# Optimization experiments

Hardware: AMD Instinct MI355X
Metric: run time of the kernel (lower is better)

## Reference

```python
import jax, jax.numpy as jnp
import numpy as np

BLOCK = 128  # block_size in the original module


def weight_dequant(weight, scale):
    # weight: [O, I] fp8 values (simulated float32); scale: [O//BLOCK, I//BLOCK] fp32
    O, I = weight.shape
    w = weight.reshape(O // BLOCK, BLOCK, I // BLOCK, BLOCK)
    w = w * scale[:, None, :, None]
    return w.reshape(O, I)


def setup_inputs() -> dict:
    key = jax.random.key(0)
    k1, k2, k3, k4 = jax.random.split(key, 4)
    B, S, IN, OUT = 2, 2048, 4096, 16384
    x = jax.random.normal(k1, (B, S, IN), dtype=jnp.float32)
    weight = jax.random.normal(k2, (OUT, IN), dtype=jnp.float32)
    scale = jax.random.uniform(k3, (OUT // BLOCK, IN // BLOCK), dtype=jnp.float32, minval=0.01, maxval=0.05)
    bias = jax.random.normal(k4, (OUT,), dtype=jnp.float32)
    return {"x": x, "weight": weight, "scale": scale, "bias": bias}


def reference(x, weight, scale, bias):
    # bf16 gemm_impl path: block-wise dequant of fp8 weight, then F.linear(x, W) + bias
    w = weight_dequant(weight, scale)          # [O, I]
    out = jnp.einsum('bsi,oi->bso', x, w)      # x @ W^T
    return out + bias
```

## Files before the change

kernel.cpp:

```cpp
#include <hip/hip_runtime.h>
#include <hip/hip_bf16.h>

#define M_DIM 4096
#define N_DIM 16384
#define K_DIM 4096

typedef __bf16 bf16x8 __attribute__((ext_vector_type(8)));
typedef float f32x4 __attribute__((ext_vector_type(4)));

__device__ __forceinline__ void gload16(const void* g, void* l) {
    __builtin_amdgcn_global_load_lds((__attribute__((address_space(1))) void*)g,
                                     (__attribute__((address_space(3))) void*)l, 16, 0, 0);
}

__global__ __launch_bounds__(256) void cvt_x_kernel(const float* __restrict__ x,
                                                    __hip_bfloat16* __restrict__ out,
                                                    int ngroups) {
    int i = blockIdx.x * blockDim.x + threadIdx.x;
    int stride = gridDim.x * blockDim.x;
    for (; i < ngroups; i += stride) {
        const float4* p = (const float4*)(x + (size_t)i * 8);
        float4 v0 = p[0];
        float4 v1 = p[1];
        bf16x8 r;
        r[0] = (__bf16)v0.x; r[1] = (__bf16)v0.y; r[2] = (__bf16)v0.z; r[3] = (__bf16)v0.w;
        r[4] = (__bf16)v1.x; r[5] = (__bf16)v1.y; r[6] = (__bf16)v1.z; r[7] = (__bf16)v1.w;
        *(bf16x8*)(out + (size_t)i * 8) = r;
    }
}

__global__ __launch_bounds__(256) void dequant_w_kernel(const float* __restrict__ w,
                                                        const float* __restrict__ scale,
                                                        __hip_bfloat16* __restrict__ out) {
    const int ngroups = N_DIM * (K_DIM / 8);
    int i = blockIdx.x * blockDim.x + threadIdx.x;
    int stride = gridDim.x * blockDim.x;
    for (; i < ngroups; i += stride) {
        int row = i >> 9;
        int cg  = i & 511;
        float s = scale[(row >> 7) * (K_DIM / 128) + (cg >> 4)];
        const float4* p = (const float4*)(w + (size_t)i * 8);
        float4 v0 = p[0];
        float4 v1 = p[1];
        bf16x8 r;
        r[0] = (__bf16)(v0.x * s); r[1] = (__bf16)(v0.y * s);
        r[2] = (__bf16)(v0.z * s); r[3] = (__bf16)(v0.w * s);
        r[4] = (__bf16)(v1.x * s); r[5] = (__bf16)(v1.y * s);
        r[6] = (__bf16)(v1.z * s); r[7] = (__bf16)(v1.w * s);
        *(bf16x8*)(out + (size_t)i * 8) = r;
    }
}

__global__ __launch_bounds__(512, 2)
void gemm_bf16_kernel(const __hip_bfloat16* __restrict__ A,
                      const __hip_bfloat16* __restrict__ Bw,
                      const float* __restrict__ bias,
                      float* __restrict__ C) {
    constexpr int Mtiles = M_DIM / 256;
    constexpr int Ntiles = N_DIM / 256;
    constexpr int nwg = Mtiles * Ntiles;
    constexpr int NT = K_DIM / 64;

    int bid = blockIdx.x;
    int swz = (bid & 7) * (nwg >> 3) + (bid >> 3);
    int bm = swz % Mtiles;
    int bn = swz / Mtiles;

    __shared__ __align__(16) __hip_bfloat16 sA[2][256 * 64];
    __shared__ __align__(16) __hip_bfloat16 sB[2][256 * 64];

    const int t = threadIdx.x;
    const int l = t & 63;
    const int w = t >> 6;
    const int wm = w >> 2;
    const int wn = w & 3;

    const int lr = l & 15;
    const int lk = l >> 4;
    const int rx = (lr & 7) << 3;

    const int srow = w * 8 + (l >> 3);
    const int scol = ((l & 7) ^ (l >> 3)) << 3;

    const size_t K = K_DIM;
    const __hip_bfloat16* aB = A  + (size_t)(bm * 256) * K;
    const __hip_bfloat16* bB = Bw + (size_t)(bn * 256) * K;

    f32x4 acc[8][4] = {};

#define STAGE(buf, kt)                                                          \
    do {                                                                        \
        const __hip_bfloat16* a0_ = aB + (kt) * 64 + scol;                      \
        const __hip_bfloat16* b0_ = bB + (kt) * 64 + scol;                      \
        char* la_ = (char*)&sA[(buf)][0] + w * 1024;                            \
        char* lb_ = (char*)&sB[(buf)][0] + w * 1024;                            \
        _Pragma("unroll")                                                       \
        for (int j = 0; j < 4; ++j) {                                           \
            gload16(a0_ + (size_t)(j * 64 + srow) * K, la_ + j * 8192);         \
            gload16(b0_ + (size_t)(j * 64 + srow) * K, lb_ + j * 8192);         \
        }                                                                       \
    } while (0)

    STAGE(0, 0);
    STAGE(1, 1);

    for (int kt = 0; kt < NT; ++kt) {
        const int cur = kt & 1;
        asm volatile("s_waitcnt vmcnt(8)" ::: "memory");
        __builtin_amdgcn_sched_barrier(0);
        __builtin_amdgcn_s_barrier();
        asm volatile("" ::: "memory");
        __builtin_amdgcn_sched_barrier(0);

        const __hip_bfloat16* pa = &sA[cur][0];
        const __hip_bfloat16* pb = &sB[cur][0];

        bf16x8 a0[4], a1[4], a2[4], a3[4], b0[4], b1[4];
        const int c0 = (lk * 8) ^ rx;
        const int c1 = (32 + lk * 8) ^ rx;

        #pragma unroll
        for (int i = 0; i < 4; ++i) {
            a0[i] = *(const bf16x8*)(pa + (wm * 128 + i * 16 + lr) * 64 + c0);
            b0[i] = *(const bf16x8*)(pb + (wn * 64  + i * 16 + lr) * 64 + c0);
        }
        #pragma unroll
        for (int i = 0; i < 4; ++i)
            a1[i] = *(const bf16x8*)(pa + (wm * 128 + 64 + i * 16 + lr) * 64 + c0);
        __builtin_amdgcn_sched_barrier(0);

        __builtin_amdgcn_s_setprio(1);
        #pragma unroll
        for (int mi = 0; mi < 4; ++mi)
            #pragma unroll
            for (int ni = 0; ni < 4; ++ni)
                acc[mi][ni] = __builtin_amdgcn_mfma_f32_16x16x32_bf16(a0[mi], b0[ni], acc[mi][ni], 0, 0, 0);
        __builtin_amdgcn_s_setprio(0);

        #pragma unroll
        for (int i = 0; i < 4; ++i) {
            a2[i] = *(const bf16x8*)(pa + (wm * 128 + i * 16 + lr) * 64 + c1);
            b1[i] = *(const bf16x8*)(pb + (wn * 64  + i * 16 + lr) * 64 + c1);
        }
        __builtin_amdgcn_sched_barrier(0);

        __builtin_amdgcn_s_setprio(1);
        #pragma unroll
        for (int mi = 0; mi < 4; ++mi)
            #pragma unroll
            for (int ni = 0; ni < 4; ++ni)
                acc[4 + mi][ni] = __builtin_amdgcn_mfma_f32_16x16x32_bf16(a1[mi], b0[ni], acc[4 + mi][ni], 0, 0, 0);
        __builtin_amdgcn_s_setprio(0);

        #pragma unroll
        for (int i = 0; i < 4; ++i)
            a3[i] = *(const bf16x8*)(pa + (wm * 128 + 64 + i * 16 + lr) * 64 + c1);
        __builtin_amdgcn_sched_barrier(0);

        __builtin_amdgcn_s_setprio(1);
        #pragma unroll
        for (int mi = 0; mi < 4; ++mi)
            #pragma unroll
            for (int ni = 0; ni < 4; ++ni)
                acc[mi][ni] = __builtin_amdgcn_mfma_f32_16x16x32_bf16(a2[mi], b1[ni], acc[mi][ni], 0, 0, 0);
        __builtin_amdgcn_s_setprio(0);
        __builtin_amdgcn_sched_barrier(0);

        __builtin_amdgcn_s_setprio(1);
        #pragma unroll
        for (int mi = 0; mi < 4; ++mi)
            #pragma unroll
            for (int ni = 0; ni < 4; ++ni)
                acc[4 + mi][ni] = __builtin_amdgcn_mfma_f32_16x16x32_bf16(a3[mi], b1[ni], acc[4 + mi][ni], 0, 0, 0);
        __builtin_amdgcn_s_setprio(0);

        __builtin_amdgcn_sched_barrier(0);
        asm volatile("s_waitcnt lgkmcnt(0)" ::: "memory");
        __builtin_amdgcn_sched_barrier(0);
        __builtin_amdgcn_s_barrier();
        asm volatile("" ::: "memory");
        __builtin_amdgcn_sched_barrier(0);
        if (kt + 2 < NT) {
            STAGE(cur, kt + 2);
        }
    }
#undef STAGE

    const int crow0 = bm * 256 + wm * 128;
    const int ccol0 = bn * 256 + wn * 64;
    #pragma unroll
    for (int ni = 0; ni < 4; ++ni) {
        int col = ccol0 + ni * 16 + lr;
        float bv = bias[col];
        #pragma unroll
        for (int mi = 0; mi < 8; ++mi) {
            int rbase = crow0 + mi * 16 + lk * 4;
            #pragma unroll
            for (int j = 0; j < 4; ++j) {
                C[(size_t)(rbase + j) * N_DIM + col] = acc[mi][ni][j] + bv;
            }
        }
    }
}

__global__ __launch_bounds__(256)
void gemm_fallback(const float* __restrict__ X, const float* __restrict__ W,
                   const float* __restrict__ scale, const float* __restrict__ bias,
                   float* __restrict__ C) {
    int bm = blockIdx.x % (M_DIM / 64);
    int bn = blockIdx.x / (M_DIM / 64);
    __shared__ float sA[64][33];
    __shared__ float sB[64][33];
    int t = threadIdx.x;
    int tx = t & 15, ty = t >> 4;
    float acc[4][4] = {};
    for (int kt = 0; kt < K_DIM / 32; ++kt) {
        float s = scale[(bn >> 1) * (K_DIM / 128) + (kt >> 2)];
        #pragma unroll
        for (int i = 0; i < 8; ++i) {
            int idx = t + i * 256;
            int r = idx >> 5, c = idx & 31;
            sA[r][c] = X[(size_t)(bm * 64 + r) * K_DIM + kt * 32 + c];
            sB[r][c] = W[(size_t)(bn * 64 + r) * K_DIM + kt * 32 + c] * s;
        }
        __syncthreads();
        #pragma unroll
        for (int k = 0; k < 32; ++k) {
            float a[4], b[4];
            #pragma unroll
            for (int i = 0; i < 4; ++i) a[i] = sA[ty * 4 + i][k];
            #pragma unroll
            for (int j = 0; j < 4; ++j) b[j] = sB[tx * 4 + j][k];
            #pragma unroll
            for (int i = 0; i < 4; ++i)
                #pragma unroll
                for (int j = 0; j < 4; ++j) acc[i][j] += a[i] * b[j];
        }
        __syncthreads();
    }
    #pragma unroll
    for (int i = 0; i < 4; ++i)
        #pragma unroll
        for (int j = 0; j < 4; ++j) {
            int row = bm * 64 + ty * 4 + i;
            int col = bn * 64 + tx * 4 + j;
            C[(size_t)row * N_DIM + col] = acc[i][j] + bias[col];
        }
}

extern "C" void kernel_launch(void* const* d_in, const int* in_sizes, int n_in,
                              void* d_out, int out_size, void* d_ws, size_t ws_size,
                              hipStream_t stream) {
    const float* x     = (const float*)d_in[0];
    const float* wgt   = (const float*)d_in[1];
    const float* scale = (const float*)d_in[2];
    const float* bias  = (const float*)d_in[3];
    float* out = (float*)d_out;

    const size_t need = ((size_t)M_DIM * K_DIM + (size_t)N_DIM * K_DIM) * sizeof(__hip_bfloat16);
    if (ws_size >= need) {
        __hip_bfloat16* xbf = (__hip_bfloat16*)d_ws;
        __hip_bfloat16* wbf = xbf + (size_t)M_DIM * K_DIM;
        cvt_x_kernel<<<2048, 256, 0, stream>>>(x, xbf, M_DIM * K_DIM / 8);
        dequant_w_kernel<<<4096, 256, 0, stream>>>(wgt, scale, wbf);
        gemm_bf16_kernel<<<(M_DIM / 256) * (N_DIM / 256), 512, 0, stream>>>(xbf, wbf, bias, out);
    } else {
        gemm_fallback<<<(M_DIM / 64) * (N_DIM / 64), 256, 0, stream>>>(x, wgt, scale, bias, out);
    }
}
```

Measured before the change: 777.6 us.

## Interleave next-tile global loads across four MFMA phases with per-phase barriers

Restructures the GEMM main loop so the global-to-LDS prefetch of tile k+1 is split into four pairs of loads. Each pair is issued between the four MFMA sub-phases of tile k, instead of staging two tiles ahead as one batch. Per-phase barriers and vmcnt waits make the prefetch overlap with compute without waiting at the end of an iteration. The cost is a prefetch distance of only one tile, four barriers per k-step instead of two, and explicit lgkmcnt waits before each MFMA group, which may expose more latency.

```diff
diff --git a/kernel.cpp b/kernel.cpp
--- a/kernel.cpp
+++ b/kernel.cpp
@@ -51,6 +51,109 @@
     }
 }
 
+template <bool ST>
+__device__ __forceinline__ void kstep(const __hip_bfloat16* __restrict__ pa,
+                                      const __hip_bfloat16* __restrict__ pb,
+                                      const __hip_bfloat16* __restrict__ aN,
+                                      const __hip_bfloat16* __restrict__ bN,
+                                      char* lAn, char* lBn,
+                                      f32x4 (&acc)[8][4],
+                                      int arow, int brow, int c0, int c1,
+                                      int srow) {
+    const size_t K = K_DIM;
+    bf16x8 av[4], bv[4], b1[4];
+
+    if (ST) {
+        gload16(bN + (size_t)(0 * 64 + srow) * K, lBn + 0 * 8192);
+        gload16(bN + (size_t)(1 * 64 + srow) * K, lBn + 1 * 8192);
+        asm volatile("s_waitcnt vmcnt(4)" ::: "memory");
+    } else {
+        asm volatile("s_waitcnt vmcnt(0)" ::: "memory");
+    }
+    __builtin_amdgcn_s_barrier();
+    __builtin_amdgcn_sched_barrier(0);
+    #pragma unroll
+    for (int i = 0; i < 4; ++i) {
+        av[i] = *(const bf16x8*)(pa + arow + i * 1024 + c0);
+        bv[i] = *(const bf16x8*)(pb + brow + i * 1024 + c0);
+    }
+    asm volatile("s_waitcnt lgkmcnt(0)" ::: "memory");
+    __builtin_amdgcn_sched_barrier(0);
+    __builtin_amdgcn_s_setprio(1);
+    #pragma unroll
+    for (int mi = 0; mi < 4; ++mi)
+        #pragma unroll
+        for (int ni = 0; ni < 4; ++ni)
+            acc[mi][ni] = __builtin_amdgcn_mfma_f32_16x16x32_bf16(av[mi], bv[ni], acc[mi][ni], 0, 0, 0);
+    __builtin_amdgcn_s_setprio(0);
+    __builtin_amdgcn_sched_barrier(0);
+
+    if (ST) {
+        gload16(bN + (size_t)(2 * 64 + srow) * K, lBn + 2 * 8192);
+        gload16(bN + (size_t)(3 * 64 + srow) * K, lBn + 3 * 8192);
+        asm volatile("s_waitcnt vmcnt(4)" ::: "memory");
+    } else {
+        asm volatile("s_waitcnt vmcnt(0)" ::: "memory");
+    }
+    __builtin_amdgcn_s_barrier();
+    __builtin_amdgcn_sched_barrier(0);
+    #pragma unroll
+    for (int i = 0; i < 4; ++i)
+        av[i] = *(const bf16x8*)(pa + arow + 4096 + i * 1024 + c0);
+    asm volatile("s_waitcnt lgkmcnt(0)" ::: "memory");
+    __builtin_amdgcn_sched_barrier(0);
+    __builtin_amdgcn_s_setprio(1);
+    #pragma unroll
+    for (int mi = 0; mi < 4; ++mi)
+        #pragma unroll
+        for (int ni = 0; ni < 4; ++ni)
+            acc[4 + mi][ni] = __builtin_amdgcn_mfma_f32_16x16x32_bf16(av[mi], bv[ni], acc[4 + mi][ni], 0, 0, 0);
+    __builtin_amdgcn_s_setprio(0);
+    __builtin_amdgcn_sched_barrier(0);
+
+    if (ST) {
+        gload16(aN + (size_t)(0 * 64 + srow) * K, lAn + 0 * 8192);
+        gload16(aN + (size_t)(2 * 64 + srow) * K, lAn + 2 * 8192);
+    }
+    __builtin_amdgcn_s_barrier();
+    __builtin_amdgcn_sched_barrier(0);
+    #pragma unroll
+    for (int i = 0; i < 4; ++i) {
+        av[i] = *(const bf16x8*)(pa + arow + i * 1024 + c1);
+        b1[i] = *(const bf16x8*)(pb + brow + i * 1024 + c1);
+    }
+    asm volatile("s_waitcnt lgkmcnt(0)" ::: "memory");
+    __builtin_amdgcn_sched_barrier(0);
+    __builtin_amdgcn_s_setprio(1);
+    #pragma unroll
+    for (int mi = 0; mi < 4; ++mi)
+        #pragma unroll
+        for (int ni = 0; ni < 4; ++ni)
+            acc[mi][ni] = __builtin_amdgcn_mfma_f32_16x16x32_bf16(av[mi], b1[ni], acc[mi][ni], 0, 0, 0);
+    __builtin_amdgcn_s_setprio(0);
+    __builtin_amdgcn_sched_barrier(0);
+
+    if (ST) {
+        gload16(aN + (size_t)(1 * 64 + srow) * K, lAn + 1 * 8192);
+        gload16(aN + (size_t)(3 * 64 + srow) * K, lAn + 3 * 8192);
+    }
+    __builtin_amdgcn_s_barrier();
+    __builtin_amdgcn_sched_barrier(0);
+    #pragma unroll
+    for (int i = 0; i < 4; ++i)
+        av[i] = *(const bf16x8*)(pa + arow + 4096 + i * 1024 + c1);
+    asm volatile("s_waitcnt lgkmcnt(0)" ::: "memory");
+    __builtin_amdgcn_sched_barrier(0);
+    __builtin_amdgcn_s_setprio(1);
+    #pragma unroll
+    for (int mi = 0; mi < 4; ++mi)
+        #pragma unroll
+        for (int ni = 0; ni < 4; ++ni)
+            acc[4 + mi][ni] = __builtin_amdgcn_mfma_f32_16x16x32_bf16(av[mi], b1[ni], acc[4 + mi][ni], 0, 0, 0);
+    __builtin_amdgcn_s_setprio(0);
+    __builtin_amdgcn_sched_barrier(0);
+}
+
 __global__ __launch_bounds__(512, 2)
 void gemm_bf16_kernel(const __hip_bfloat16* __restrict__ A,
                       const __hip_bfloat16* __restrict__ Bw,
@@ -83,108 +186,44 @@
     const int scol = ((l & 7) ^ (l >> 3)) << 3;
 
     const size_t K = K_DIM;
-    const __hip_bfloat16* aB = A  + (size_t)(bm * 256) * K;
-    const __hip_bfloat16* bB = Bw + (size_t)(bn * 256) * K;
+    const __hip_bfloat16* aB = A  + (size_t)(bm * 256) * K + scol;
+    const __hip_bfloat16* bB = Bw + (size_t)(bn * 256) * K + scol;
 
     f32x4 acc[8][4] = {};
 
-#define STAGE(buf, kt)                                                          \
-    do {                                                                        \
-        const __hip_bfloat16* a0_ = aB + (kt) * 64 + scol;                      \
-        const __hip_bfloat16* b0_ = bB + (kt) * 64 + scol;                      \
-        char* la_ = (char*)&sA[(buf)][0] + w * 1024;                            \
-        char* lb_ = (char*)&sB[(buf)][0] + w * 1024;                            \
-        _Pragma("unroll")                                                       \
-        for (int j = 0; j < 4; ++j) {                                           \
-            gload16(a0_ + (size_t)(j * 64 + srow) * K, la_ + j * 8192);         \
-            gload16(b0_ + (size_t)(j * 64 + srow) * K, lb_ + j * 8192);         \
-        }                                                                       \
-    } while (0)
-
-    STAGE(0, 0);
-    STAGE(1, 1);
-
-    for (int kt = 0; kt < NT; ++kt) {
+    const int c0 = (lk * 8) ^ rx;
+    const int c1 = (32 + lk * 8) ^ rx;
+    const int arow = (wm * 128 + lr) * 64;
+    const int brow = (wn * 64 + lr) * 64;
+
+    {
+        char* la_ = (char*)&sA[0][0] + w * 1024;
+        char* lb_ = (char*)&sB[0][0] + w * 1024;
+        #pragma unroll
+        for (int j = 0; j < 4; ++j) {
+            gload16(aB + (size_t)(j * 64 + srow) * K, la_ + j * 8192);
+            gload16(bB + (size_t)(j * 64 + srow) * K, lb_ + j * 8192);
+        }
+    }
+    asm volatile("s_waitcnt vmcnt(0)" ::: "memory");
+    __builtin_amdgcn_s_barrier();
+    __builtin_amdgcn_sched_barrier(0);
+
+    for (int kt = 0; kt + 1 < NT; ++kt) {
         const int cur = kt & 1;
-        asm volatile("s_waitcnt vmcnt(8)" ::: "memory");
-        __builtin_amdgcn_sched_barrier(0);
-        __builtin_amdgcn_s_barrier();
-        asm volatile("" ::: "memory");
-        __builtin_amdgcn_sched_barrier(0);
-
-        const __hip_bfloat16* pa = &sA[cur][0];
-        const __hip_bfloat16* pb = &sB[cur][0];
-
-        bf16x8 a0[4], a1[4], a2[4], a3[4], b0[4], b1[4];
-        const int c0 = (lk * 8) ^ rx;
-        const int c1 = (32 + lk * 8) ^ rx;
-
-        #pragma unroll
-        for (int i = 0; i < 4; ++i) {
-            a0[i] = *(const bf16x8*)(pa + (wm * 128 + i * 16 + lr) * 64 + c0);
-            b0[i] = *(const bf16x8*)(pb + (wn * 64  + i * 16 + lr) * 64 + c0);
-        }
-        #pragma unroll
-        for (int i = 0; i < 4; ++i)
-            a1[i] = *(const bf16x8*)(pa + (wm * 128 + 64 + i * 16 + lr) * 64 + c0);
-        __builtin_amdgcn_sched_barrier(0);
-
-        __builtin_amdgcn_s_setprio(1);
-        #pragma unroll
-        for (int mi = 0; mi < 4; ++mi)
-            #pragma unroll
-            for (int ni = 0; ni < 4; ++ni)
-                acc[mi][ni] = __builtin_amdgcn_mfma_f32_16x16x32_bf16(a0[mi], b0[ni], acc[mi][ni], 0, 0, 0);
-        __builtin_amdgcn_s_setprio(0);
-
-        #pragma unroll
-        for (int i = 0; i < 4; ++i) {
-            a2[i] = *(const bf16x8*)(pa + (wm * 128 + i * 16 + lr) * 64 + c1);
-            b1[i] = *(const bf16x8*)(pb + (wn * 64  + i * 16 + lr) * 64 + c1);
-        }
-        __builtin_amdgcn_sched_barrier(0);
-
-        __builtin_amdgcn_s_setprio(1);
-        #pragma unroll
-        for (int mi = 0; mi < 4; ++mi)
-            #pragma unroll
-            for (int ni = 0; ni < 4; ++ni)
-                acc[4 + mi][ni] = __builtin_amdgcn_mfma_f32_16x16x32_bf16(a1[mi], b0[ni], acc[4 + mi][ni], 0, 0, 0);
-        __builtin_amdgcn_s_setprio(0);
-
-        #pragma unroll
-        for (int i = 0; i < 4; ++i)
-            a3[i] = *(const bf16x8*)(pa + (wm * 128 + 64 + i * 16 + lr) * 64 + c1);
-        __builtin_amdgcn_sched_barrier(0);
-
-        __builtin_amdgcn_s_setprio(1);
-        #pragma unroll
-        for (int mi = 0; mi < 4; ++mi)
-            #pragma unroll
-            for (int ni = 0; ni < 4; ++ni)
-                acc[mi][ni] = __builtin_amdgcn_mfma_f32_16x16x32_bf16(a2[mi], b1[ni], acc[mi][ni], 0, 0, 0);
-        __builtin_amdgcn_s_setprio(0);
-        __builtin_amdgcn_sched_barrier(0);
-
-        __builtin_amdgcn_s_setprio(1);
-        #pragma unroll
-        for (int mi = 0; mi < 4; ++mi)
-            #pragma unroll
-            for (int ni = 0; ni < 4; ++ni)
-                acc[4 + mi][ni] = __builtin_amdgcn_mfma_f32_16x16x32_bf16(a3[mi], b1[ni], acc[4 + mi][ni], 0, 0, 0);
-        __builtin_amdgcn_s_setprio(0);
-
-        __builtin_amdgcn_sched_barrier(0);
-        asm volatile("s_waitcnt lgkmcnt(0)" ::: "memory");
-        __builtin_amdgcn_sched_barrier(0);
-        __builtin_amdgcn_s_barrier();
-        asm volatile("" ::: "memory");
-        __builtin_amdgcn_sched_barrier(0);
-        if (kt + 2 < NT) {
-            STAGE(cur, kt + 2);
-        }
-    }
-#undef STAGE
+        kstep<true>(&sA[cur][0], &sB[cur][0],
+                    aB + (kt + 1) * 64, bB + (kt + 1) * 64,
+                    (char*)&sA[cur ^ 1][0] + w * 1024,
+                    (char*)&sB[cur ^ 1][0] + w * 1024,
+                    acc, arow, brow, c0, c1, srow);
+    }
+    {
+        const int cur = (NT - 1) & 1;
+        kstep<false>(&sA[cur][0], &sB[cur][0], aB, bB,
+                     (char*)&sA[cur ^ 1][0] + w * 1024,
+                     (char*)&sB[cur ^ 1][0] + w * 1024,
+                     acc, arow, brow, c0, c1, srow);
+    }
 
     const int crow0 = bm * 256 + wm * 128;
     const int ccol0 = bn * 256 + wn * 64;
```

Result: slower. 806.0 us (+3.7%).

## Software-pipeline LDS fragment loads across MFMA clusters and k-iterations

Applied to the files above, without the earlier changes.

Restructures the GEMM main loop so LDS fragment reads are issued ahead of the MFMA cluster that consumes them, using partial lgkmcnt waits instead of draining before each block of math. The next tile's first A/B fragments are prefetched from the other LDS buffer before the last MFMA cluster of the current iteration, and the refill of the freed buffer is issued there too. Register reuse (aE/aO/bL/bH) replaces the six separate fragment arrays, and the loop is kept rolled. The intent is to hide LDS latency and cut barrier stalls, at the cost of a stricter vmcnt(0) wait and an extra barrier per iteration.

```diff
diff --git a/kernel.cpp b/kernel.cpp
--- a/kernel.cpp
+++ b/kernel.cpp
@@ -83,108 +83,123 @@
     const int scol = ((l & 7) ^ (l >> 3)) << 3;
 
     const size_t K = K_DIM;
-    const __hip_bfloat16* aB = A  + (size_t)(bm * 256) * K;
-    const __hip_bfloat16* bB = Bw + (size_t)(bn * 256) * K;
+    const __hip_bfloat16* aB = A  + (size_t)(bm * 256) * K + scol;
+    const __hip_bfloat16* bB = Bw + (size_t)(bn * 256) * K + scol;
 
     f32x4 acc[8][4] = {};
 
-#define STAGE(buf, kt)                                                          \
+    const int c0 = (lk * 8) ^ rx;
+    const int c1 = (32 + lk * 8) ^ rx;
+    const int arow = (wm * 128 + lr) * 64;
+    const int brow = (wn * 64 + lr) * 64;
+
+#define STAGE(bufidx, gA, gBp)                                                  \
     do {                                                                        \
-        const __hip_bfloat16* a0_ = aB + (kt) * 64 + scol;                      \
-        const __hip_bfloat16* b0_ = bB + (kt) * 64 + scol;                      \
-        char* la_ = (char*)&sA[(buf)][0] + w * 1024;                            \
-        char* lb_ = (char*)&sB[(buf)][0] + w * 1024;                            \
+        char* la_ = (char*)&sA[(bufidx)][0] + w * 1024;                         \
+        char* lb_ = (char*)&sB[(bufidx)][0] + w * 1024;                         \
         _Pragma("unroll")                                                       \
         for (int j = 0; j < 4; ++j) {                                           \
-            gload16(a0_ + (size_t)(j * 64 + srow) * K, la_ + j * 8192);         \
-            gload16(b0_ + (size_t)(j * 64 + srow) * K, lb_ + j * 8192);         \
+            gload16((gA) + (size_t)(j * 64 + srow) * K, la_ + j * 8192);        \
+            gload16((gBp) + (size_t)(j * 64 + srow) * K, lb_ + j * 8192);       \
         }                                                                       \
     } while (0)
 
-    STAGE(0, 0);
-    STAGE(1, 1);
-
+#define CLUSTER(af, bf, off)                                                    \
+    do {                                                                        \
+        __builtin_amdgcn_s_setprio(1);                                          \
+        _Pragma("unroll")                                                       \
+        for (int mi = 0; mi < 4; ++mi)                                          \
+            _Pragma("unroll")                                                   \
+            for (int ni = 0; ni < 4; ++ni)                                      \
+                acc[(off) + mi][ni] = __builtin_amdgcn_mfma_f32_16x16x32_bf16(  \
+                    af[mi], bf[ni], acc[(off) + mi][ni], 0, 0, 0);              \
+        __builtin_amdgcn_s_setprio(0);                                          \
+    } while (0)
+
+    bf16x8 aE[4], aO[4], bL[4], bH[4];
+    const __hip_bfloat16* pa;
+    const __hip_bfloat16* pb;
+
+    STAGE(0, aB, bB);
+    STAGE(1, aB + 64, bB + 64);
+    asm volatile("s_waitcnt vmcnt(8)" ::: "memory");
+    __builtin_amdgcn_sched_barrier(0);
+    __builtin_amdgcn_s_barrier();
+    __builtin_amdgcn_sched_barrier(0);
+    pa = &sA[0][0];
+    pb = &sB[0][0];
+    #pragma unroll
+    for (int i = 0; i < 4; ++i) {
+        aE[i] = *(const bf16x8*)(pa + arow + i * 1024 + c0);
+        bL[i] = *(const bf16x8*)(pb + brow + i * 1024 + c0);
+    }
+    __builtin_amdgcn_sched_barrier(0);
+
+    #pragma unroll 1
     for (int kt = 0; kt < NT; ++kt) {
         const int cur = kt & 1;
-        asm volatile("s_waitcnt vmcnt(8)" ::: "memory");
-        __builtin_amdgcn_sched_barrier(0);
-        __builtin_amdgcn_s_barrier();
-        asm volatile("" ::: "memory");
-        __builtin_amdgcn_sched_barrier(0);
-
-        const __hip_bfloat16* pa = &sA[cur][0];
-        const __hip_bfloat16* pb = &sB[cur][0];
-
-        bf16x8 a0[4], a1[4], a2[4], a3[4], b0[4], b1[4];
-        const int c0 = (lk * 8) ^ rx;
-        const int c1 = (32 + lk * 8) ^ rx;
+        pa = &sA[cur][0];
+        pb = &sB[cur][0];
+        const __hip_bfloat16* paN = &sA[cur ^ 1][0];
+        const __hip_bfloat16* pbN = &sB[cur ^ 1][0];
+
+        #pragma unroll
+        for (int i = 0; i < 4; ++i)
+            aO[i] = *(const bf16x8*)(pa + arow + 4096 + i * 1024 + c0);
+        __builtin_amdgcn_sched_barrier(0);
+        asm volatile("s_waitcnt lgkmcnt(4)" ::: "memory");
+        __builtin_amdgcn_sched_barrier(0);
+        CLUSTER(aE, bL, 0);
+        __builtin_amdgcn_sched_barrier(0);
 
         #pragma unroll
         for (int i = 0; i < 4; ++i) {
-            a0[i] = *(const bf16x8*)(pa + (wm * 128 + i * 16 + lr) * 64 + c0);
-            b0[i] = *(const bf16x8*)(pb + (wn * 64  + i * 16 + lr) * 64 + c0);
-        }
+            aE[i] = *(const bf16x8*)(pa + arow + i * 1024 + c1);
+            bH[i] = *(const bf16x8*)(pb + brow + i * 1024 + c1);
+        }
+        __builtin_amdgcn_sched_barrier(0);
+        asm volatile("s_waitcnt lgkmcnt(8)" ::: "memory");
+        __builtin_amdgcn_sched_barrier(0);
+        CLUSTER(aO, bL, 4);
+        __builtin_amdgcn_sched_barrier(0);
+
         #pragma unroll
         for (int i = 0; i < 4; ++i)
-            a1[i] = *(const bf16x8*)(pa + (wm * 128 + 64 + i * 16 + lr) * 64 + c0);
-        __builtin_amdgcn_sched_barrier(0);
-
-        __builtin_amdgcn_s_setprio(1);
-        #pragma unroll
-        for (int mi = 0; mi < 4; ++mi)
-            #pragma unroll
-            for (int ni = 0; ni < 4; ++ni)
-                acc[mi][ni] = __builtin_amdgcn_mfma_f32_16x16x32_bf16(a0[mi], b0[ni], acc[mi][ni], 0, 0, 0);
-        __builtin_amdgcn_s_setprio(0);
-
-        #pragma unroll
-        for (int i = 0; i < 4; ++i) {
-            a2[i] = *(const bf16x8*)(pa + (wm * 128 + i * 16 + lr) * 64 + c1);
-            b1[i] = *(const bf16x8*)(pb + (wn * 64  + i * 16 + lr) * 64 + c1);
-        }
-        __builtin_amdgcn_sched_barrier(0);
-
-        __builtin_amdgcn_s_setprio(1);
-        #pragma unroll
-        for (int mi = 0; mi < 4; ++mi)
-            #pragma unroll
-            for (int ni = 0; ni < 4; ++ni)
-                acc[4 + mi][ni] = __builtin_amdgcn_mfma_f32_16x16x32_bf16(a1[mi], b0[ni], acc[4 + mi][ni], 0, 0, 0);
-        __builtin_amdgcn_s_setprio(0);
-
-        #pragma unroll
-        for (int i = 0; i < 4; ++i)
-            a3[i] = *(const bf16x8*)(pa + (wm * 128 + 64 + i * 16 + lr) * 64 + c1);
-        __builtin_amdgcn_sched_barrier(0);
-
-        __builtin_amdgcn_s_setprio(1);
-        #pragma unroll
-        for (int mi = 0; mi < 4; ++mi)
-            #pragma unroll
-            for (int ni = 0; ni < 4; ++ni)
-                acc[mi][ni] = __builtin_amdgcn_mfma_f32_16x16x32_bf16(a2[mi], b1[ni], acc[mi][ni], 0, 0, 0);
-        __builtin_amdgcn_s_setprio(0);
-        __builtin_amdgcn_sched_barrier(0);
-
-        __builtin_amdgcn_s_setprio(1);
-        #pragma unroll
-        for (int mi = 0; mi < 4; ++mi)
-            #pragma unroll
-            for (int ni = 0; ni < 4; ++ni)
-                acc[4 + mi][ni] = __builtin_amdgcn_mfma_f32_16x16x32_bf16(a3[mi], b1[ni], acc[4 + mi][ni], 0, 0, 0);
-        __builtin_amdgcn_s_setprio(0);
-
-        __builtin_amdgcn_sched_barrier(0);
-        asm volatile("s_waitcnt lgkmcnt(0)" ::: "memory");
-        __builtin_amdgcn_sched_barrier(0);
-        __builtin_amdgcn_s_barrier();
-        asm volatile("" ::: "memory");
-        __builtin_amdgcn_sched_barrier(0);
-        if (kt + 2 < NT) {
-            STAGE(cur, kt + 2);
-        }
+            aO[i] = *(const bf16x8*)(pa + arow + 4096 + i * 1024 + c1);
+        __builtin_amdgcn_sched_barrier(0);
+        asm volatile("s_waitcnt lgkmcnt(4)" ::: "memory");
+        __builtin_amdgcn_sched_barrier(0);
+        CLUSTER(aE, bH, 0);
+        __builtin_amdgcn_sched_barrier(0);
+
+        if (kt + 1 < NT) {
+            asm volatile("s_waitcnt vmcnt(0)" ::: "memory");
+            __builtin_amdgcn_sched_barrier(0);
+            __builtin_amdgcn_s_barrier();
+            __builtin_amdgcn_sched_barrier(0);
+            #pragma unroll
+            for (int i = 0; i < 4; ++i) {
+                aE[i] = *(const bf16x8*)(paN + arow + i * 1024 + c0);
+                bL[i] = *(const bf16x8*)(pbN + brow + i * 1024 + c0);
+            }
+            __builtin_amdgcn_sched_barrier(0);
+            asm volatile("s_waitcnt lgkmcnt(8)" ::: "memory");
+            __builtin_amdgcn_sched_barrier(0);
+            __builtin_amdgcn_s_barrier();
+            __builtin_amdgcn_sched_barrier(0);
+            if (kt + 2 < NT) {
+                STAGE(cur, aB + (kt + 2) * 64, bB + (kt + 2) * 64);
+            }
+            __builtin_amdgcn_sched_barrier(0);
+        } else {
+            asm volatile("s_waitcnt lgkmcnt(0)" ::: "memory");
+            __builtin_amdgcn_sched_barrier(0);
+        }
+        CLUSTER(aO, bH, 4);
+        __builtin_amdgcn_sched_barrier(0);
     }
 #undef STAGE
+#undef CLUSTER
 
     const int crow0 = bm * 256 + wm * 128;
     const int ccol0 = bn * 256 + wn * 64;
```

Measured after the change: 779.9 us. No clear change (+0.3%).
